# Kernel optimization log

Hardware: AMD Instinct MI355X
Metric: run time of the kernel (lower is better)

Reference implementation:

```python
import jax, jax.numpy as jnp
import numpy as np

N_EMBD = 1024
N_HEAD = 16
HEAD_DIM = N_EMBD // N_HEAD


def setup_inputs() -> dict:
    key = jax.random.key(0)
    k1, k2, k3, k4, k5 = jax.random.split(key, 5)
    B, T, C = 4, 2048, N_EMBD
    s = 1.0 / np.sqrt(C)
    return {
        "x": jax.random.normal(k1, (B, T, C), dtype=jnp.float32),
        "W_attn": jax.random.normal(k2, (C, 3 * C), dtype=jnp.float32) * s,
        "b_attn": jnp.zeros((3 * C,), dtype=jnp.float32),
        "W_proj": jax.random.normal(k3, (C, C), dtype=jnp.float32) * s,
        "b_proj": jnp.zeros((C,), dtype=jnp.float32),
    }


def reference(x, W_attn, b_attn, W_proj, b_proj):
    B, T, C = x.shape
    H, D = N_HEAD, HEAD_DIM
    # fused QKV projection
    qkv = x @ W_attn + b_attn                       # [B,T,3C]
    q, k, v = jnp.split(qkv, 3, axis=2)
    q = q.reshape(B, T, H, D).transpose(0, 2, 1, 3)  # [B,H,T,D]
    k = k.reshape(B, T, H, D).transpose(0, 2, 1, 3)
    v = v.reshape(B, T, H, D).transpose(0, 2, 1, 3)
    # causal scaled dot-product attention
    scale = 1.0 / jnp.sqrt(jnp.asarray(D, dtype=x.dtype))
    scores = jnp.einsum('bhqd,bhkd->bhqk', q, k) * scale  # [B,H,T,T]
    causal = jnp.tril(jnp.ones((T, T), dtype=bool))
    scores = jnp.where(causal[None, None], scores, jnp.finfo(x.dtype).min)
    attn = jax.nn.softmax(scores, axis=-1)
    y = jnp.einsum('bhqk,bhkd->bhqd', attn, v)      # [B,H,T,D]
    y = y.transpose(0, 2, 1, 3).reshape(B, T, C)
    return y @ W_proj + b_proj
```

## Files before the change

kernel.cpp:

```cpp
#include <hip/hip_runtime.h>
#include <hip/hip_bf16.h>
#include <cstdint>

#define B_ 4
#define T_ 2048
#define C_ 1024
#define H_ 16
#define D_ 64
#define M_ (B_*T_)
#define N3 (3*C_)

typedef __bf16 bf16;
typedef __bf16 bf16x8 __attribute__((ext_vector_type(8)));
typedef __bf16 bf16x4 __attribute__((ext_vector_type(4)));
typedef float  floatx4 __attribute__((ext_vector_type(4)));

__device__ __forceinline__ void gl_lds16(const bf16* g, bf16* l) {
  __builtin_amdgcn_global_load_lds(
      (__attribute__((address_space(1))) void*)(void*)g,
      (__attribute__((address_space(3))) void*)(void*)l,
      16, 0, 0);
}

__global__ void cast_to_bf16(const float* __restrict__ in, bf16* __restrict__ out, int n) {
  int i = (blockIdx.x * blockDim.x + threadIdx.x) * 4;
  if (i < n) {
    const float4 f = *(const float4*)(in + i);
    bf16x4 o;
    o.x = (bf16)f.x; o.y = (bf16)f.y; o.z = (bf16)f.z; o.w = (bf16)f.w;
    *(bf16x4*)(out + i) = o;
  }
}

__global__ void transpose_cast(const float* __restrict__ in, bf16* __restrict__ out,
                               int R, int C) {
  __shared__ float tile[32][33];
  int r0 = blockIdx.y * 32, c0 = blockIdx.x * 32;
  int tx = threadIdx.x & 31, ty = threadIdx.x >> 5;
  #pragma unroll
  for (int j = 0; j < 32; j += 8)
    tile[ty + j][tx] = in[(size_t)(r0 + ty + j) * C + c0 + tx];
  __syncthreads();
  #pragma unroll
  for (int j = 0; j < 32; j += 8)
    out[(size_t)(c0 + ty + j) * R + r0 + tx] = (bf16)tile[tx][ty + j];
}

__global__ __launch_bounds__(256)
void transpose_v(const bf16* __restrict__ in, bf16* __restrict__ out) {
  __shared__ __attribute__((aligned(16))) bf16 tileN[64 * 64];
  const int tid = threadIdx.x;
  const int bh = blockIdx.z;
  const int t0 = blockIdx.x * 64;
  const int sk = tid >> 2, scc = tid & 3;
  {
    const bf16* p = in + ((size_t)bh * T_ + t0 + sk) * D_ + scc * 16;
    const bf16x8 r0 = *(const bf16x8*)p;
    const bf16x8 r1 = *(const bf16x8*)(p + 8);
    *(bf16x8*)(tileN + sk * 64 + ((2 * scc)     ^ (sk & 7)) * 8) = r0;
    *(bf16x8*)(tileN + sk * 64 + ((2 * scc + 1) ^ (sk & 7)) * 8) = r1;
  }
  __syncthreads();
  const int tc = (tid & 7) * 8;
  #pragma unroll
  for (int half = 0; half < 2; half++) {
    const int d = (tid >> 3) + half * 32;
    bf16x8 o;
    #pragma unroll
    for (int j = 0; j < 8; j++) {
      const int slot = tc + j;
      const int row = 16 * (slot & 3) + (slot >> 2);
      o[j] = tileN[row * 64 + (((d >> 3) ^ (row & 7)) * 8) + (d & 7)];
    }
    *(bf16x8*)(out + ((size_t)bh * D_ + d) * T_ + t0 + tc) = o;
  }
}

template<int MODE>
__global__ __launch_bounds__(256)
void gemm_bt(const bf16* __restrict__ A, const bf16* __restrict__ Bt,
             const float* __restrict__ bias, float* __restrict__ out,
             bf16* __restrict__ qo, bf16* __restrict__ ko, bf16* __restrict__ vo,
             int M, int N, int K)
{
  __shared__ __attribute__((aligned(16))) bf16 As[128 * 32];
  __shared__ __attribute__((aligned(16))) bf16 Bs[128 * 32];

  const int tid  = threadIdx.x;
  const int w    = tid >> 6;
  const int lane = tid & 63;
  const int quad = lane >> 4;
  const int l16  = lane & 15;
  const int wm   = w & 1, wn = w >> 1;
  const int m0   = blockIdx.y * 128, n0 = blockIdx.x * 128;

  floatx4 acc[4][4] = {};

  const int lrow = lane >> 2;
  const int lk   = (lane & 3) * 8;

  const bf16* aptr = A  + (size_t)(m0 + w * 32 + lrow) * K + lk;
  const bf16* bptr = Bt + (size_t)(n0 + w * 32 + lrow) * K + lk;
  bf16* asl = As + w * 1024;
  bf16* bsl = Bs + w * 1024;

  for (int k0 = 0; k0 < K; k0 += 32) {
    gl_lds16(aptr,          asl);
    gl_lds16(aptr + 16 * K, asl + 512);
    gl_lds16(bptr,          bsl);
    gl_lds16(bptr + 16 * K, bsl + 512);
    aptr += 32; bptr += 32;
    __syncthreads();

    bf16x8 af[4], bfb[4];
    #pragma unroll
    for (int i = 0; i < 4; i++)
      af[i] = *(const bf16x8*)(As + (wm * 64 + i * 16 + l16) * 32 + quad * 8);
    #pragma unroll
    for (int i = 0; i < 4; i++)
      bfb[i] = *(const bf16x8*)(Bs + (wn * 64 + i * 16 + l16) * 32 + quad * 8);
    #pragma unroll
    for (int mi = 0; mi < 4; mi++)
      #pragma unroll
      for (int ni = 0; ni < 4; ni++)
        acc[mi][ni] = __builtin_amdgcn_mfma_f32_16x16x32_bf16(af[mi], bfb[ni], acc[mi][ni], 0, 0, 0);
    __syncthreads();
  }

  #pragma unroll
  for (int mi = 0; mi < 4; mi++) {
    #pragma unroll
    for (int ni = 0; ni < 4; ni++) {
      const int col = n0 + wn * 64 + ni * 16 + l16;
      const float bv = bias[col];
      #pragma unroll
      for (int r = 0; r < 4; r++) {
        const int row = m0 + wm * 64 + mi * 16 + quad * 4 + r;
        const float val = acc[mi][ni][r] + bv;
        if (MODE == 0) {
          const int b = row >> 11, t = row & 2047;
          const int s = col >> 10, c = col & 1023;
          const int h = c >> 6,  d = c & 63;
          bf16* dst = (s == 0) ? qo : (s == 1) ? ko : vo;
          dst[((size_t)(b * H_ + h) * T_ + t) * D_ + d] = (bf16)val;
        } else {
          out[(size_t)row * N + col] = val;
        }
      }
    }
  }
}

__global__ __launch_bounds__(256)
void attn_kernel(const bf16* __restrict__ Q, const bf16* __restrict__ Kp,
                 const bf16* __restrict__ Vtp, bf16* __restrict__ Y)
{
  __shared__ __attribute__((aligned(16))) bf16 Ks[2][64 * 72];
  __shared__ __attribute__((aligned(16))) bf16 Vs[2][64 * 72];
  __shared__ __attribute__((aligned(16))) bf16 Ps[4][16 * 72];

  const int tid  = threadIdx.x;
  const int w    = tid >> 6, lane = tid & 63;
  const int quad = lane >> 4, l16 = lane & 15;
  const int bh = blockIdx.y;
  const int b = bh >> 4, h = bh & 15;

  const int sk = tid >> 2;
  const int sc = (tid & 3) * 16;

  const bf16* Kbase = Kp  + (size_t)bh * T_ * D_;
  const bf16* Vbase = Vtp + (size_t)bh * D_ * T_;

  const float SC = 0.125f * 1.44269504088896f;

  #pragma unroll 1
  for (int tix = 0; tix < 2; tix++) {
    const int qt = (tix == 0) ? (15 - (int)blockIdx.x) : (int)blockIdx.x;
    const int q0 = qt * 128;
    const int nch = 2 * qt + 2;

    bf16x8 qf[2][2];
    #pragma unroll
    for (int mt = 0; mt < 2; mt++) {
      const bf16* qp = Q + ((size_t)bh * T_ + q0 + mt * 64 + w * 16 + l16) * D_ + quad * 8;
      qf[mt][0] = *(const bf16x8*)qp;
      qf[mt][1] = *(const bf16x8*)(qp + 32);
    }

    floatx4 o[2][4] = {};
    float l_r[2][4] = {};

    {
      const bf16* kp = Kbase + (size_t)sk * D_ + sc;
      const bf16x8 k0 = *(const bf16x8*)kp, k1 = *(const bf16x8*)(kp + 8);
      const bf16* vp = Vbase + (size_t)sk * T_ + sc;
      const bf16x8 v0 = *(const bf16x8*)vp, v1 = *(const bf16x8*)(vp + 8);
      bf16* kd = Ks[0] + sk * 72 + sc;
      *(bf16x8*)kd = k0; *(bf16x8*)(kd + 8) = k1;
      bf16* vd = Vs[0] + sk * 72 + sc;
      *(bf16x8*)vd = v0; *(bf16x8*)(vd + 8) = v1;
    }
    __syncthreads();

    #pragma unroll 1
    for (int c = 0; c < nch; c++) {
      const int cur = c & 1;

      bf16x8 nk0, nk1, nv0, nv1;
      const bool have = (c + 1 < nch);
      if (have) {
        const bf16* kp = Kbase + (size_t)((c + 1) * 64 + sk) * D_ + sc;
        nk0 = *(const bf16x8*)kp; nk1 = *(const bf16x8*)(kp + 8);
        const bf16* vp = Vbase + (size_t)sk * T_ + (c + 1) * 64 + sc;
        nv0 = *(const bf16x8*)vp; nv1 = *(const bf16x8*)(vp + 8);
      }

      const bf16* KsC = Ks[cur];
      const bf16* VsC = Vs[cur];
      const int kv0 = c * 64;
      const bool act0 = (c < nch - 1);

      floatx4 s[2][4];
      #pragma unroll
      for (int nt = 0; nt < 4; nt++) {
        const bf16x8 kf0 = *(const bf16x8*)(KsC + (nt * 16 + l16) * 72 + quad * 8);
        const bf16x8 kf1 = *(const bf16x8*)(KsC + (nt * 16 + l16) * 72 + 32 + quad * 8);
        if (act0) {
          floatx4 z = {};
          z = __builtin_amdgcn_mfma_f32_16x16x32_bf16(qf[0][0], kf0, z, 0, 0, 0);
          s[0][nt] = __builtin_amdgcn_mfma_f32_16x16x32_bf16(qf[0][1], kf1, z, 0, 0, 0);
        }
        floatx4 z = {};
        z = __builtin_amdgcn_mfma_f32_16x16x32_bf16(qf[1][0], kf0, z, 0, 0, 0);
        s[1][nt] = __builtin_amdgcn_mfma_f32_16x16x32_bf16(qf[1][1], kf1, z, 0, 0, 0);
      }

      bf16x8 vfr[4][2];
      #pragma unroll
      for (int nt = 0; nt < 4; nt++) {
        vfr[nt][0] = *(const bf16x8*)(VsC + (nt * 16 + l16) * 72 + quad * 8);
        vfr[nt][1] = *(const bf16x8*)(VsC + (nt * 16 + l16) * 72 + 32 + quad * 8);
      }

      #pragma unroll
      for (int mt = 0; mt < 2; mt++) {
        if (mt == 0 && !act0) continue;
        const bool diag = (c == 2 * qt + mt);
        #pragma unroll
        for (int r = 0; r < 4; r++) {
          const int qrow = q0 + mt * 64 + w * 16 + quad * 4 + r;
          float x0 = s[mt][0][r], x1 = s[mt][1][r], x2 = s[mt][2][r], x3 = s[mt][3][r];
          if (diag) {
            if (kv0      + l16 > qrow) x0 = -1e30f;
            if (kv0 + 16 + l16 > qrow) x1 = -1e30f;
            if (kv0 + 32 + l16 > qrow) x2 = -1e30f;
            if (kv0 + 48 + l16 > qrow) x3 = -1e30f;
          }
          const float e0 = exp2f(fmaf(x0, SC, -8.f));
          const float e1 = exp2f(fmaf(x1, SC, -8.f));
          const float e2 = exp2f(fmaf(x2, SC, -8.f));
          const float e3 = exp2f(fmaf(x3, SC, -8.f));
          l_r[mt][r] += (e0 + e1) + (e2 + e3);
          bf16x4 pv;
          pv.x = (bf16)e0; pv.y = (bf16)e1; pv.z = (bf16)e2; pv.w = (bf16)e3;
          *(bf16x4*)(&Ps[w][(quad * 4 + r) * 72 + l16 * 4]) = pv;
        }
        const bf16x8 pf0 = *(const bf16x8*)(&Ps[w][l16 * 72 + quad * 8]);
        const bf16x8 pf1 = *(const bf16x8*)(&Ps[w][l16 * 72 + 32 + quad * 8]);
        #pragma unroll
        for (int nt = 0; nt < 4; nt++) {
          o[mt][nt] = __builtin_amdgcn_mfma_f32_16x16x32_bf16(pf0, vfr[nt][0], o[mt][nt], 0, 0, 0);
          o[mt][nt] = __builtin_amdgcn_mfma_f32_16x16x32_bf16(pf1, vfr[nt][1], o[mt][nt], 0, 0, 0);
        }
      }

      if (have) {
        bf16* kd = Ks[cur ^ 1] + sk * 72 + sc;
        *(bf16x8*)kd = nk0; *(bf16x8*)(kd + 8) = nk1;
        bf16* vd = Vs[cur ^ 1] + sk * 72 + sc;
        *(bf16x8*)vd = nv0; *(bf16x8*)(vd + 8) = nv1;
      }
      __syncthreads();
    }

    #pragma unroll
    for (int mt = 0; mt < 2; mt++) {
      #pragma unroll
      for (int r = 0; r < 4; r++) {
        float ls = l_r[mt][r];
        ls += __shfl_xor(ls, 1);
        ls += __shfl_xor(ls, 2);
        ls += __shfl_xor(ls, 4);
        ls += __shfl_xor(ls, 8);
        const float inv = 1.f / ls;
        const int t = q0 + mt * 64 + w * 16 + quad * 4 + r;
        #pragma unroll
        for (int nt = 0; nt < 4; nt++)
          Y[((size_t)b * T_ + t) * C_ + h * D_ + nt * 16 + l16] = (bf16)(o[mt][nt][r] * inv);
      }
    }
  }
}

extern "C" void kernel_launch(void* const* d_in, const int* in_sizes, int n_in,
                              void* d_out, int out_size, void* d_ws, size_t ws_size,
                              hipStream_t stream)
{
  const float* x      = (const float*)d_in[0];
  const float* W_attn = (const float*)d_in[1];
  const float* b_attn = (const float*)d_in[2];
  const float* W_proj = (const float*)d_in[3];
  const float* b_proj = (const float*)d_in[4];
  float* out = (float*)d_out;

  bf16* xb  = (bf16*)d_ws;
  bf16* wat = xb  + (size_t)M_ * C_;
  bf16* wpt = wat + (size_t)N3 * C_;
  bf16* qb  = wpt + (size_t)C_ * C_;
  bf16* kb  = qb  + (size_t)M_ * C_;
  bf16* vb  = kb  + (size_t)M_ * C_;
  bf16* yb  = vb  + (size_t)M_ * C_;
  bf16* vtb = xb;

  cast_to_bf16<<<dim3(M_ * C_ / 1024), 256, 0, stream>>>(x, xb, M_ * C_);
  transpose_cast<<<dim3(N3 / 32, C_ / 32), 256, 0, stream>>>(W_attn, wat, C_, N3);
  transpose_cast<<<dim3(C_ / 32, C_ / 32), 256, 0, stream>>>(W_proj, wpt, C_, C_);
  gemm_bt<0><<<dim3(N3 / 128, M_ / 128), 256, 0, stream>>>(
      xb, wat, b_attn, nullptr, qb, kb, vb, M_, N3, C_);
  transpose_v<<<dim3(T_ / 64, 1, B_ * H_), 256, 0, stream>>>(vb, vtb);
  attn_kernel<<<dim3(T_ / 256, B_ * H_), 256, 0, stream>>>(qb, kb, vtb, yb);
  gemm_bt<1><<<dim3(C_ / 128, M_ / 128), 256, 0, stream>>>(
      yb, wpt, b_proj, out, nullptr, nullptr, nullptr, M_, C_, C_);
}
```

Baseline: 293.2 us.

## Launch one attention block per query tile, longest-first, with fast exp2 and truncating bf16 pack

The attention kernel no longer pairs two query tiles (long and short) inside one block. Instead it launches 16 q-tiles by 64 heads, one tile per block, with the grid ordered so the heaviest causal tiles are dispatched first. This doubles the block count to improve occupancy and load balance across CUs. It also switches exp2f to the hardware exp2 intrinsic, packs probabilities to bf16 by truncation instead of rounding, and uses incrementing K/V pointers, which slightly lowers precision.

```diff
diff --git a/kernel.cpp b/kernel.cpp
--- a/kernel.cpp
+++ b/kernel.cpp
@@ -20,6 +20,12 @@
       (__attribute__((address_space(1))) void*)(void*)g,
       (__attribute__((address_space(3))) void*)(void*)l,
       16, 0, 0);
+}
+
+__device__ __forceinline__ uint32_t pack_bf16_trunc(float lo, float hi) {
+  union { float f; uint32_t u; } a, b;
+  a.f = lo; b.f = hi;
+  return (a.u >> 16) | (b.u & 0xffff0000u);
 }
 
 __global__ void cast_to_bf16(const float* __restrict__ in, bf16* __restrict__ out, int n) {
@@ -162,142 +168,137 @@
   const int tid  = threadIdx.x;
   const int w    = tid >> 6, lane = tid & 63;
   const int quad = lane >> 4, l16 = lane & 15;
-  const int bh = blockIdx.y;
+  const int bh = blockIdx.x;
   const int b = bh >> 4, h = bh & 15;
+  const int qt = 15 - (int)blockIdx.y;
+  const int q0 = qt * 128;
+  const int nch = 2 * qt + 2;
 
   const int sk = tid >> 2;
   const int sc = (tid & 3) * 16;
 
-  const bf16* Kbase = Kp  + (size_t)bh * T_ * D_;
-  const bf16* Vbase = Vtp + (size_t)bh * D_ * T_;
-
   const float SC = 0.125f * 1.44269504088896f;
 
+  bf16x8 qf[2][2];
+  #pragma unroll
+  for (int mt = 0; mt < 2; mt++) {
+    const bf16* qp = Q + ((size_t)bh * T_ + q0 + mt * 64 + w * 16 + l16) * D_ + quad * 8;
+    qf[mt][0] = *(const bf16x8*)qp;
+    qf[mt][1] = *(const bf16x8*)(qp + 32);
+  }
+
+  floatx4 o[2][4] = {};
+  float l_r[2][4] = {};
+
+  const bf16* kpp = Kp  + (size_t)bh * T_ * D_ + (size_t)sk * D_ + sc;
+  const bf16* vpp = Vtp + (size_t)bh * D_ * T_ + (size_t)sk * T_ + sc;
+
+  {
+    const bf16x8 k0 = *(const bf16x8*)kpp, k1 = *(const bf16x8*)(kpp + 8);
+    const bf16x8 v0 = *(const bf16x8*)vpp, v1 = *(const bf16x8*)(vpp + 8);
+    bf16* kd = Ks[0] + sk * 72 + sc;
+    *(bf16x8*)kd = k0; *(bf16x8*)(kd + 8) = k1;
+    bf16* vd = Vs[0] + sk * 72 + sc;
+    *(bf16x8*)vd = v0; *(bf16x8*)(vd + 8) = v1;
+    kpp += 64 * D_; vpp += 64;
+  }
+  __syncthreads();
+
   #pragma unroll 1
-  for (int tix = 0; tix < 2; tix++) {
-    const int qt = (tix == 0) ? (15 - (int)blockIdx.x) : (int)blockIdx.x;
-    const int q0 = qt * 128;
-    const int nch = 2 * qt + 2;
-
-    bf16x8 qf[2][2];
+  for (int c = 0; c < nch; c++) {
+    const int cur = c & 1;
+
+    bf16x8 nk0, nk1, nv0, nv1;
+    const bool have = (c + 1 < nch);
+    if (have) {
+      nk0 = *(const bf16x8*)kpp; nk1 = *(const bf16x8*)(kpp + 8);
+      nv0 = *(const bf16x8*)vpp; nv1 = *(const bf16x8*)(vpp + 8);
+      kpp += 64 * D_; vpp += 64;
+    }
+
+    const bf16* KsC = Ks[cur];
+    const bf16* VsC = Vs[cur];
+    const int kv0 = c * 64;
+    const bool act0 = (c < nch - 1);
+
+    floatx4 s[2][4];
+    #pragma unroll
+    for (int nt = 0; nt < 4; nt++) {
+      const bf16x8 kf0 = *(const bf16x8*)(KsC + (nt * 16 + l16) * 72 + quad * 8);
+      const bf16x8 kf1 = *(const bf16x8*)(KsC + (nt * 16 + l16) * 72 + 32 + quad * 8);
+      if (act0) {
+        floatx4 z = {};
+        z = __builtin_amdgcn_mfma_f32_16x16x32_bf16(qf[0][0], kf0, z, 0, 0, 0);
+        s[0][nt] = __builtin_amdgcn_mfma_f32_16x16x32_bf16(qf[0][1], kf1, z, 0, 0, 0);
+      }
+      floatx4 z = {};
+      z = __builtin_amdgcn_mfma_f32_16x16x32_bf16(qf[1][0], kf0, z, 0, 0, 0);
+      s[1][nt] = __builtin_amdgcn_mfma_f32_16x16x32_bf16(qf[1][1], kf1, z, 0, 0, 0);
+    }
+
+    bf16x8 vfr[4][2];
+    #pragma unroll
+    for (int nt = 0; nt < 4; nt++) {
+      vfr[nt][0] = *(const bf16x8*)(VsC + (nt * 16 + l16) * 72 + quad * 8);
+      vfr[nt][1] = *(const bf16x8*)(VsC + (nt * 16 + l16) * 72 + 32 + quad * 8);
+    }
+
     #pragma unroll
     for (int mt = 0; mt < 2; mt++) {
-      const bf16* qp = Q + ((size_t)bh * T_ + q0 + mt * 64 + w * 16 + l16) * D_ + quad * 8;
-      qf[mt][0] = *(const bf16x8*)qp;
-      qf[mt][1] = *(const bf16x8*)(qp + 32);
-    }
-
-    floatx4 o[2][4] = {};
-    float l_r[2][4] = {};
-
-    {
-      const bf16* kp = Kbase + (size_t)sk * D_ + sc;
-      const bf16x8 k0 = *(const bf16x8*)kp, k1 = *(const bf16x8*)(kp + 8);
-      const bf16* vp = Vbase + (size_t)sk * T_ + sc;
-      const bf16x8 v0 = *(const bf16x8*)vp, v1 = *(const bf16x8*)(vp + 8);
-      bf16* kd = Ks[0] + sk * 72 + sc;
-      *(bf16x8*)kd = k0; *(bf16x8*)(kd + 8) = k1;
-      bf16* vd = Vs[0] + sk * 72 + sc;
-      *(bf16x8*)vd = v0; *(bf16x8*)(vd + 8) = v1;
+      if (mt == 0 && !act0) continue;
+      const bool diag = (c == 2 * qt + mt);
+      #pragma unroll
+      for (int r = 0; r < 4; r++) {
+        const int qrow = q0 + mt * 64 + w * 16 + quad * 4 + r;
+        float x0 = s[mt][0][r], x1 = s[mt][1][r], x2 = s[mt][2][r], x3 = s[mt][3][r];
+        if (diag) {
+          if (kv0      + l16 > qrow) x0 = -1e30f;
+          if (kv0 + 16 + l16 > qrow) x1 = -1e30f;
+          if (kv0 + 32 + l16 > qrow) x2 = -1e30f;
+          if (kv0 + 48 + l16 > qrow) x3 = -1e30f;
+        }
+        const float e0 = __builtin_amdgcn_exp2f(fmaf(x0, SC, -8.f));
+        const float e1 = __builtin_amdgcn_exp2f(fmaf(x1, SC, -8.f));
+        const float e2 = __builtin_amdgcn_exp2f(fmaf(x2, SC, -8.f));
+        const float e3 = __builtin_amdgcn_exp2f(fmaf(x3, SC, -8.f));
+        l_r[mt][r] += (e0 + e1) + (e2 + e3);
+        uint2 pk;
+        pk.x = pack_bf16_trunc(e0, e1);
+        pk.y = pack_bf16_trunc(e2, e3);
+        *(uint2*)(&Ps[w][(quad * 4 + r) * 72 + l16 * 4]) = pk;
+      }
+      const bf16x8 pf0 = *(const bf16x8*)(&Ps[w][l16 * 72 + quad * 8]);
+      const bf16x8 pf1 = *(const bf16x8*)(&Ps[w][l16 * 72 + 32 + quad * 8]);
+      #pragma unroll
+      for (int nt = 0; nt < 4; nt++) {
+        o[mt][nt] = __builtin_amdgcn_mfma_f32_16x16x32_bf16(pf0, vfr[nt][0], o[mt][nt], 0, 0, 0);
+        o[mt][nt] = __builtin_amdgcn_mfma_f32_16x16x32_bf16(pf1, vfr[nt][1], o[mt][nt], 0, 0, 0);
+      }
+    }
+
+    if (have) {
+      bf16* kd = Ks[cur ^ 1] + sk * 72 + sc;
+      *(bf16x8*)kd = nk0; *(bf16x8*)(kd + 8) = nk1;
+      bf16* vd = Vs[cur ^ 1] + sk * 72 + sc;
+      *(bf16x8*)vd = nv0; *(bf16x8*)(vd + 8) = nv1;
     }
     __syncthreads();
-
-    #pragma unroll 1
-    for (int c = 0; c < nch; c++) {
-      const int cur = c & 1;
-
-      bf16x8 nk0, nk1, nv0, nv1;
-      const bool have = (c + 1 < nch);
-      if (have) {
-        const bf16* kp = Kbase + (size_t)((c + 1) * 64 + sk) * D_ + sc;
-        nk0 = *(const bf16x8*)kp; nk1 = *(const bf16x8*)(kp + 8);
-        const bf16* vp = Vbase + (size_t)sk * T_ + (c + 1) * 64 + sc;
-        nv0 = *(const bf16x8*)vp; nv1 = *(const bf16x8*)(vp + 8);
-      }
-
-      const bf16* KsC = Ks[cur];
-      const bf16* VsC = Vs[cur];
-      const int kv0 = c * 64;
-      const bool act0 = (c < nch - 1);
-
-      floatx4 s[2][4];
-      #pragma unroll
-      for (int nt = 0; nt < 4; nt++) {
-        const bf16x8 kf0 = *(const bf16x8*)(KsC + (nt * 16 + l16) * 72 + quad * 8);
-        const bf16x8 kf1 = *(const bf16x8*)(KsC + (nt * 16 + l16) * 72 + 32 + quad * 8);
-        if (act0) {
-          floatx4 z = {};
-          z = __builtin_amdgcn_mfma_f32_16x16x32_bf16(qf[0][0], kf0, z, 0, 0, 0);
-          s[0][nt] = __builtin_amdgcn_mfma_f32_16x16x32_bf16(qf[0][1], kf1, z, 0, 0, 0);
-        }
-        floatx4 z = {};
-        z = __builtin_amdgcn_mfma_f32_16x16x32_bf16(qf[1][0], kf0, z, 0, 0, 0);
-        s[1][nt] = __builtin_amdgcn_mfma_f32_16x16x32_bf16(qf[1][1], kf1, z, 0, 0, 0);
-      }
-
-      bf16x8 vfr[4][2];
-      #pragma unroll
-      for (int nt = 0; nt < 4; nt++) {
-        vfr[nt][0] = *(const bf16x8*)(VsC + (nt * 16 + l16) * 72 + quad * 8);
-        vfr[nt][1] = *(const bf16x8*)(VsC + (nt * 16 + l16) * 72 + 32 + quad * 8);
-      }
-
-      #pragma unroll
-      for (int mt = 0; mt < 2; mt++) {
-        if (mt == 0 && !act0) continue;
-        const bool diag = (c == 2 * qt + mt);
-        #pragma unroll
-        for (int r = 0; r < 4; r++) {
-          const int qrow = q0 + mt * 64 + w * 16 + quad * 4 + r;
-          float x0 = s[mt][0][r], x1 = s[mt][1][r], x2 = s[mt][2][r], x3 = s[mt][3][r];
-          if (diag) {
-            if (kv0      + l16 > qrow) x0 = -1e30f;
-            if (kv0 + 16 + l16 > qrow) x1 = -1e30f;
-            if (kv0 + 32 + l16 > qrow) x2 = -1e30f;
-            if (kv0 + 48 + l16 > qrow) x3 = -1e30f;
-          }
-          const float e0 = exp2f(fmaf(x0, SC, -8.f));
-          const float e1 = exp2f(fmaf(x1, SC, -8.f));
-          const float e2 = exp2f(fmaf(x2, SC, -8.f));
-          const float e3 = exp2f(fmaf(x3, SC, -8.f));
-          l_r[mt][r] += (e0 + e1) + (e2 + e3);
-          bf16x4 pv;
-          pv.x = (bf16)e0; pv.y = (bf16)e1; pv.z = (bf16)e2; pv.w = (bf16)e3;
-          *(bf16x4*)(&Ps[w][(quad * 4 + r) * 72 + l16 * 4]) = pv;
-        }
-        const bf16x8 pf0 = *(const bf16x8*)(&Ps[w][l16 * 72 + quad * 8]);
-        const bf16x8 pf1 = *(const bf16x8*)(&Ps[w][l16 * 72 + 32 + quad * 8]);
-        #pragma unroll
-        for (int nt = 0; nt < 4; nt++) {
-          o[mt][nt] = __builtin_amdgcn_mfma_f32_16x16x32_bf16(pf0, vfr[nt][0], o[mt][nt], 0, 0, 0);
-          o[mt][nt] = __builtin_amdgcn_mfma_f32_16x16x32_bf16(pf1, vfr[nt][1], o[mt][nt], 0, 0, 0);
-        }
-      }
-
-      if (have) {
-        bf16* kd = Ks[cur ^ 1] + sk * 72 + sc;
-        *(bf16x8*)kd = nk0; *(bf16x8*)(kd + 8) = nk1;
-        bf16* vd = Vs[cur ^ 1] + sk * 72 + sc;
-        *(bf16x8*)vd = nv0; *(bf16x8*)(vd + 8) = nv1;
-      }
-      __syncthreads();
-    }
-
-    #pragma unroll
-    for (int mt = 0; mt < 2; mt++) {
-      #pragma unroll
-      for (int r = 0; r < 4; r++) {
-        float ls = l_r[mt][r];
-        ls += __shfl_xor(ls, 1);
-        ls += __shfl_xor(ls, 2);
-        ls += __shfl_xor(ls, 4);
-        ls += __shfl_xor(ls, 8);
-        const float inv = 1.f / ls;
-        const int t = q0 + mt * 64 + w * 16 + quad * 4 + r;
-        #pragma unroll
-        for (int nt = 0; nt < 4; nt++)
-          Y[((size_t)b * T_ + t) * C_ + h * D_ + nt * 16 + l16] = (bf16)(o[mt][nt][r] * inv);
-      }
+  }
+
+  #pragma unroll
+  for (int mt = 0; mt < 2; mt++) {
+    #pragma unroll
+    for (int r = 0; r < 4; r++) {
+      float ls = l_r[mt][r];
+      ls += __shfl_xor(ls, 1);
+      ls += __shfl_xor(ls, 2);
+      ls += __shfl_xor(ls, 4);
+      ls += __shfl_xor(ls, 8);
+      const float inv = 1.f / ls;
+      const int t = q0 + mt * 64 + w * 16 + quad * 4 + r;
+      #pragma unroll
+      for (int nt = 0; nt < 4; nt++)
+        Y[((size_t)b * T_ + t) * C_ + h * D_ + nt * 16 + l16] = (bf16)(o[mt][nt][r] * inv);
     }
   }
 }
@@ -328,7 +329,7 @@
   gemm_bt<0><<<dim3(N3 / 128, M_ / 128), 256, 0, stream>>>(
       xb, wat, b_attn, nullptr, qb, kb, vb, M_, N3, C_);
   transpose_v<<<dim3(T_ / 64, 1, B_ * H_), 256, 0, stream>>>(vb, vtb);
-  attn_kernel<<<dim3(T_ / 256, B_ * H_), 256, 0, stream>>>(qb, kb, vtb, yb);
+  attn_kernel<<<dim3(B_ * H_, 16), 256, 0, stream>>>(qb, kb, vtb, yb);
   gemm_bt<1><<<dim3(C_ / 128, M_ / 128), 256, 0, stream>>>(
       yb, wpt, b_proj, out, nullptr, nullptr, nullptr, M_, C_, C_);
 }
```

New measurement: 268.5 us. 1.09x faster.
